# Optimization experiments

Measured on AMD Instinct MI355X. Metric: run time of the kernel, lower is better.

## Reference

```python
import jax, jax.numpy as jnp
import numpy as np

N_NODES = 50000
N_EDGES = 1600000
D = 128
LEAKY_SLOPE = 0.01  # torch nn.LeakyReLU default


def setup_inputs() -> dict:
    key = jax.random.key(0)
    ks = jax.random.split(key, 7)
    entity_embed = jax.random.normal(ks[0], (N_NODES, D), dtype=jnp.float32)
    W1 = jax.random.normal(ks[1], (D, D), dtype=jnp.float32) * 0.05
    b1 = jax.random.normal(ks[2], (D,), dtype=jnp.float32) * 0.05
    W2 = jax.random.normal(ks[3], (D, D), dtype=jnp.float32) * 0.05
    b2 = jax.random.normal(ks[4], (D,), dtype=jnp.float32) * 0.05
    src = jax.random.randint(ks[5], (N_EDGES,), 0, N_NODES, dtype=jnp.int32)
    dst = jax.random.randint(ks[6], (N_EDGES,), 0, N_NODES, dtype=jnp.int32)
    return {"entity_embed": entity_embed, "W1": W1, "b1": b1,
            "W2": W2, "b2": b2, "src": src, "dst": dst}


def reference(entity_embed, W1, b1, W2, b2, src, dst):
    # DGL update_all(copy_u('node','side'), sum('side','H')):
    # H[v] = sum over edges (u -> v) of entity_embed[u]
    n = entity_embed.shape[0]
    H = jax.ops.segment_sum(entity_embed[src], dst, num_segments=n)  # [N, D]
    # neighbors branch: LeakyReLU(W_1 @ H)
    neighbors = jax.nn.leaky_relu(H @ W1.T + b1, negative_slope=LEAKY_SLOPE)
    # interactions branch: LeakyReLU(W_2 @ (node * H))
    interactions = jax.nn.leaky_relu((entity_embed * H) @ W2.T + b2,
                                     negative_slope=LEAKY_SLOPE)
    # dropout is identity at inference
    return neighbors + interactions
```

## Files before the change

### kernel.cpp

```cpp
#include <hip/hip_runtime.h>

#define NN 50000
#define DD 128
#define SLOPE 0.01f
#define NB 782
#define BCAP 2560
#define ECH 6144
#define BST 512
#define PB 2
#define OVCAP 8192
#define HP 136

using bf16x8 = __attribute__((ext_vector_type(8))) short;
using f32x4  = __attribute__((ext_vector_type(4))) float;

__device__ inline float bflo(unsigned int w) { return __uint_as_float(w << 16); }
__device__ inline float bfhi(unsigned int w) { return __uint_as_float(w & 0xffff0000u); }
__device__ inline float sbf(short s) {
    return __uint_as_float(((unsigned int)(unsigned short)s) << 16);
}
__device__ inline unsigned int rnebf(float f) {
    unsigned int u = __float_as_uint(f);
    return (u + 0x7fffu + ((u >> 16) & 1u)) >> 16;
}
__device__ inline unsigned int pack2(float lo, float hi) {
    return rnebf(lo) | (rnebf(hi) << 16);
}
__device__ inline uint4 pack8f(const float* f) {
    uint4 o;
    o.x = pack2(f[0], f[1]); o.y = pack2(f[2], f[3]);
    o.z = pack2(f[4], f[5]); o.w = pack2(f[6], f[7]);
    return o;
}
__device__ inline void addrow(float* acc, uint4 r) {
    acc[0] += bflo(r.x); acc[1] += bfhi(r.x);
    acc[2] += bflo(r.y); acc[3] += bfhi(r.y);
    acc[4] += bflo(r.z); acc[5] += bfhi(r.z);
    acc[6] += bflo(r.w); acc[7] += bfhi(r.w);
}

__global__ __launch_bounds__(BST) void convert_bin(
    const float* __restrict__ E, const float* __restrict__ W1,
    const float* __restrict__ W2, const int* __restrict__ src,
    const int* __restrict__ dst, unsigned short* __restrict__ Ebf,
    unsigned short* __restrict__ W1b, unsigned short* __restrict__ W2b,
    int* __restrict__ gtail, unsigned int* __restrict__ stag,
    int* __restrict__ ovf_cnt, int2* __restrict__ ovf,
    int n_edges, int nbin)
{
    const int tid = threadIdx.x;

    if (blockIdx.x >= nbin) {
        const int NE8 = NN * DD / 8;
        const int NW8 = DD * DD / 8;
        int t = (blockIdx.x - nbin) * BST + tid;
        const float* s; unsigned short* d; int idx;
        if (t < NE8)                { s = E;  d = Ebf; idx = t; }
        else if (t < NE8 + NW8)     { s = W1; d = W1b; idx = t - NE8; }
        else if (t < NE8 + 2 * NW8) { s = W2; d = W2b; idx = t - NE8 - NW8; }
        else return;
        float4 a = ((const float4*)s)[(size_t)idx * 2];
        float4 b = ((const float4*)s)[(size_t)idx * 2 + 1];
        uint4 o;
        o.x = pack2(a.x, a.y); o.y = pack2(a.z, a.w);
        o.z = pack2(b.x, b.y); o.w = pack2(b.z, b.w);
        ((uint4*)d)[idx] = o;
        return;
    }

    __shared__ unsigned int srt[ECH];
    __shared__ int cnt[NB], off[NB], pos[NB], gbase[NB];
    __shared__ int wsum[BST / 64];

    const int e0 = blockIdx.x * ECH;
    const int m = min(ECH, n_edges - e0);

    for (int b = tid; b < NB; b += BST) cnt[b] = 0;
    __syncthreads();

    for (int i = tid; i < m; i += BST)
        atomicAdd(&cnt[dst[e0 + i] >> 6], 1);
    __syncthreads();

    const int lane = tid & 63, w = tid >> 6;
    int b0 = tid * PB;
    int loc[PB]; int s = 0;
    #pragma unroll
    for (int j = 0; j < PB; ++j) {
        int bb = b0 + j;
        int cv = (bb < NB) ? cnt[bb] : 0;
        loc[j] = s; s += cv;
    }
    int incl = s;
    #pragma unroll
    for (int d = 1; d < 64; d <<= 1) {
        int t2 = __shfl_up(incl, d);
        if (lane >= d) incl += t2;
    }
    if (lane == 63) wsum[w] = incl;
    __syncthreads();
    int wbase = 0;
    for (int w2 = 0; w2 < w; ++w2) wbase += wsum[w2];
    int base = wbase + incl - s;
    #pragma unroll
    for (int j = 0; j < PB; ++j) {
        int bb = b0 + j;
        if (bb < NB) { off[bb] = base + loc[j]; pos[bb] = base + loc[j]; }
    }
    __syncthreads();

    for (int i = tid; i < m; i += BST) {
        int v = dst[e0 + i];
        int u = src[e0 + i];
        int bb = v >> 6;
        int p = atomicAdd(&pos[bb], 1);
        srt[p] = (unsigned int)u | ((unsigned int)(v & 63) << 16)
               | ((unsigned int)bb << 22);
    }
    __syncthreads();

    for (int bb = tid; bb < NB; bb += BST) {
        int c = cnt[bb];
        if (c) gbase[bb] = atomicAdd(&gtail[bb], c);
    }
    __syncthreads();

    for (int i = tid; i < m; i += BST) {
        unsigned int r = srt[i];
        int bb = (int)(r >> 22);
        int gp = gbase[bb] + (i - off[bb]);
        if (gp < BCAP) {
            stag[(size_t)bb * BCAP + gp] = r & 0x3fffffu;
        } else {
            int oi = atomicAdd(ovf_cnt, 1);
            if (oi < OVCAP)
                ovf[oi] = make_int2((int)(r & 0xffffu),
                                    bb * 64 + (int)((r >> 16) & 63));
        }
    }
}

__global__ __launch_bounds__(512) void bucket_fused(
    const unsigned short* __restrict__ Ebf, const int* __restrict__ gtail,
    const unsigned int* __restrict__ stag, const int* __restrict__ ovf_cnt,
    const int2* __restrict__ ovf,
    const unsigned short* __restrict__ W1b, const unsigned short* __restrict__ W2b,
    const float* __restrict__ b1, const float* __restrict__ b2,
    float* __restrict__ out)
{
    __shared__ unsigned short sorted[BCAP];
    __shared__ unsigned short Hs[64][HP];
    __shared__ int cnt[64], off[65], pos[64];
    __shared__ int s_novf;

    const int b = blockIdx.x;
    const int tid = threadIdx.x;
    int len = gtail[b]; len = len < BCAP ? len : BCAP;
    const unsigned int* seg = stag + (size_t)b * BCAP;

    if (tid == 0) { int t = *ovf_cnt; s_novf = t < OVCAP ? t : OVCAP; }
    if (tid < 64) cnt[tid] = 0;
    __syncthreads();
    for (int i = tid; i < len; i += 512)
        atomicAdd(&cnt[(seg[i] >> 16) & 63], 1);
    __syncthreads();
    if (tid == 0) {
        int a = 0;
        for (int j = 0; j < 64; ++j) { off[j] = a; pos[j] = a; a += cnt[j]; }
        off[64] = a;
    }
    __syncthreads();
    for (int i = tid; i < len; i += 512) {
        unsigned int r = seg[i];
        int p = atomicAdd(&pos[(r >> 16) & 63], 1);
        sorted[p] = (unsigned short)(r & 0xffffu);
    }
    __syncthreads();
    const int novf = s_novf;

    const int g = tid >> 4;
    const int c = tid & 15;
    const uint4* E4 = (const uint4*)Ebf;
    for (int p2 = 0; p2 < 2; ++p2) {
        int nl = p2 * 32 + g;
        int v = b * 64 + nl;
        if (v >= NN) continue;
        float acc[8] = {};
        int i = off[nl], e1 = off[nl + 1];
        for (; i + 8 <= e1; i += 8) {
            uint4 r0 = E4[(size_t)sorted[i]     * 16 + c];
            uint4 r1 = E4[(size_t)sorted[i + 1] * 16 + c];
            uint4 r2 = E4[(size_t)sorted[i + 2] * 16 + c];
            uint4 r3 = E4[(size_t)sorted[i + 3] * 16 + c];
            uint4 r4 = E4[(size_t)sorted[i + 4] * 16 + c];
            uint4 r5 = E4[(size_t)sorted[i + 5] * 16 + c];
            uint4 r6 = E4[(size_t)sorted[i + 6] * 16 + c];
            uint4 r7 = E4[(size_t)sorted[i + 7] * 16 + c];
            addrow(acc, r0); addrow(acc, r1); addrow(acc, r2); addrow(acc, r3);
            addrow(acc, r4); addrow(acc, r5); addrow(acc, r6); addrow(acc, r7);
        }
        for (; i + 2 <= e1; i += 2) {
            uint4 r0 = E4[(size_t)sorted[i]     * 16 + c];
            uint4 r1 = E4[(size_t)sorted[i + 1] * 16 + c];
            addrow(acc, r0); addrow(acc, r1);
        }
        if (i < e1) addrow(acc, E4[(size_t)sorted[i] * 16 + c]);

        if (novf > 0) {
            for (int k = 0; k < novf; ++k) {
                int2 e = ovf[k];
                if (e.y == v) addrow(acc, E4[(size_t)e.x * 16 + c]);
            }
        }
        *(uint4*)&Hs[nl][c * 8] = pack8f(acc);
    }
    __syncthreads();

    const int wave = tid >> 6;
    const int lane = tid & 63;
    const int rw = wave >> 1;
    const int ch = wave & 1;
    const int v0 = b * 64 + rw * 16;
    if (v0 >= NN) return;
    const int m = lane & 15;
    const int quad = lane >> 4;

    bf16x8 aH[4], aE[4];
    const unsigned short* hrow = &Hs[rw * 16 + m][quad * 8];
    const unsigned short* erow = Ebf + (size_t)(v0 + m) * DD + quad * 8;
    #pragma unroll
    for (int ks = 0; ks < 4; ++ks) {
        bf16x8 h8 = *(const bf16x8*)(hrow + ks * 32);
        bf16x8 e8 = *(const bf16x8*)(erow + ks * 32);
        aH[ks] = h8;
        bf16x8 eh;
        #pragma unroll
        for (int j = 0; j < 8; ++j)
            eh[j] = (short)rnebf(sbf(h8[j]) * sbf(e8[j]));
        aE[ks] = eh;
    }

    #pragma unroll
    for (int jt = ch * 4; jt < ch * 4 + 4; ++jt) {
        const int j0 = jt * 16;
        const unsigned short* w1r = W1b + (size_t)(j0 + m) * DD + quad * 8;
        const unsigned short* w2r = W2b + (size_t)(j0 + m) * DD + quad * 8;
        f32x4 acc1 = {0.f, 0.f, 0.f, 0.f}, acc2 = {0.f, 0.f, 0.f, 0.f};
        #pragma unroll
        for (int ks = 0; ks < 4; ++ks) {
            bf16x8 bw1 = *(const bf16x8*)(w1r + ks * 32);
            bf16x8 bw2 = *(const bf16x8*)(w2r + ks * 32);
            acc1 = __builtin_amdgcn_mfma_f32_16x16x32_bf16(aH[ks], bw1, acc1, 0, 0, 0);
            acc2 = __builtin_amdgcn_mfma_f32_16x16x32_bf16(aE[ks], bw2, acc2, 0, 0, 0);
        }
        const float bb1 = b1[j0 + m], bb2 = b2[j0 + m];
        #pragma unroll
        for (int i = 0; i < 4; ++i) {
            int row = v0 + quad * 4 + i;
            if (row < NN) {
                float x1 = acc1[i] + bb1; x1 = x1 > 0.f ? x1 : SLOPE * x1;
                float x2 = acc2[i] + bb2; x2 = x2 > 0.f ? x2 : SLOPE * x2;
                out[(size_t)row * DD + j0 + m] = x1 + x2;
            }
        }
    }
}

__global__ __launch_bounds__(256) void scatter_add(
    const float* __restrict__ E, const int* __restrict__ src,
    const int* __restrict__ dst, float* __restrict__ H, int n_edges)
{
    int t = blockIdx.x * 256 + threadIdx.x;
    int e = t >> 5;
    if (e >= n_edges) return;
    int c = t & 31;
    float4 a = ((const float4*)E)[(size_t)src[e] * 32 + c];
    float* hp = H + (size_t)dst[e] * DD + c * 4;
    atomicAdd(hp + 0, a.x); atomicAdd(hp + 1, a.y);
    atomicAdd(hp + 2, a.z); atomicAdd(hp + 3, a.w);
}

__global__ __launch_bounds__(256) void fused_mlp(
    const float* __restrict__ E, const float* __restrict__ H,
    const float* __restrict__ W1, const float* __restrict__ b1,
    const float* __restrict__ W2, const float* __restrict__ b2,
    float* __restrict__ out)
{
    __shared__ float Hsf[32][DD];
    __shared__ float EHs[32][DD];
    __shared__ float W1s[DD][20];
    __shared__ float W2s[DD][20];
    const int tid = threadIdx.x;
    const int v0 = blockIdx.x * 32;
    const int nvalid = min(32, NN - v0);
    for (int i = 0; i < 4; ++i) {
        int f = tid + 256 * i;
        int n = f >> 5, c = f & 31;
        float4 h = make_float4(0.f, 0.f, 0.f, 0.f);
        float4 eh = h;
        if (n < nvalid) {
            h = ((const float4*)H)[(size_t)(v0 + n) * 32 + c];
            float4 e4 = ((const float4*)E)[(size_t)(v0 + n) * 32 + c];
            eh = make_float4(e4.x * h.x, e4.y * h.y, e4.z * h.z, e4.w * h.w);
        }
        *((float4*)&Hsf[n][c * 4]) = h;
        *((float4*)&EHs[n][c * 4]) = eh;
    }
    const int jg = tid & 63;
    const int n0 = (tid >> 6) * 8;
    float acc1a[8] = {}, acc1b[8] = {}, acc2a[8] = {}, acc2b[8] = {};
    for (int t8 = 0; t8 < 8; ++t8) {
        const int k0 = t8 * 16;
        __syncthreads();
        for (int i = 0; i < 8; ++i) {
            int f = tid + 256 * i;
            int j = f >> 4, kk = f & 15;
            W1s[j][kk] = W1[j * DD + k0 + kk];
            W2s[j][kk] = W2[j * DD + k0 + kk];
        }
        __syncthreads();
        for (int c = 0; c < 4; ++c) {
            float4 w1a = *((const float4*)&W1s[jg][c * 4]);
            float4 w1b = *((const float4*)&W1s[jg + 64][c * 4]);
            float4 w2a = *((const float4*)&W2s[jg][c * 4]);
            float4 w2b = *((const float4*)&W2s[jg + 64][c * 4]);
            const int kk = k0 + c * 4;
            for (int n = 0; n < 8; ++n) {
                float4 h = *((const float4*)&Hsf[n0 + n][kk]);
                float4 eh = *((const float4*)&EHs[n0 + n][kk]);
                acc1a[n] += h.x * w1a.x + h.y * w1a.y + h.z * w1a.z + h.w * w1a.w;
                acc1b[n] += h.x * w1b.x + h.y * w1b.y + h.z * w1b.z + h.w * w1b.w;
                acc2a[n] += eh.x * w2a.x + eh.y * w2a.y + eh.z * w2a.z + eh.w * w2a.w;
                acc2b[n] += eh.x * w2b.x + eh.y * w2b.y + eh.z * w2b.z + eh.w * w2b.w;
            }
        }
    }
    const float b1a = b1[jg], b1b = b1[jg + 64];
    const float b2a = b2[jg], b2b = b2[jg + 64];
    for (int n = 0; n < 8; ++n) {
        if (n0 + n < nvalid) {
            const int v = v0 + n0 + n;
            float x1 = acc1a[n] + b1a; x1 = x1 > 0.f ? x1 : SLOPE * x1;
            float x2 = acc2a[n] + b2a; x2 = x2 > 0.f ? x2 : SLOPE * x2;
            out[(size_t)v * DD + jg] = x1 + x2;
            float y1 = acc1b[n] + b1b; y1 = y1 > 0.f ? y1 : SLOPE * y1;
            float y2 = acc2b[n] + b2b; y2 = y2 > 0.f ? y2 : SLOPE * y2;
            out[(size_t)v * DD + jg + 64] = y1 + y2;
        }
    }
}

extern "C" void kernel_launch(void* const* d_in, const int* in_sizes, int n_in,
                              void* d_out, int out_size, void* d_ws, size_t ws_size,
                              hipStream_t stream)
{
    const float* E  = (const float*)d_in[0];
    const float* W1 = (const float*)d_in[1];
    const float* b1 = (const float*)d_in[2];
    const float* W2 = (const float*)d_in[3];
    const float* b2 = (const float*)d_in[4];
    const int* src  = (const int*)d_in[5];
    const int* dst  = (const int*)d_in[6];
    float* out = (float*)d_out;
    const int n_edges = in_sizes[5];

    char* ws = (char*)d_ws;
    auto al = [](size_t x) { return (x + 255) & ~(size_t)255; };

    const size_t off_tail = 0;
    const size_t off_ovfc = (size_t)NB * 4;
    const size_t off_ovf  = al(off_ovfc + 4);
    const size_t off_stag = al(off_ovf + (size_t)OVCAP * 8);
    const size_t off_Ebf  = al(off_stag + (size_t)NB * BCAP * 4);
    const size_t off_W1b  = al(off_Ebf + (size_t)NN * DD * 2);
    const size_t off_W2b  = al(off_W1b + (size_t)DD * DD * 2);
    const size_t need_bf  = off_W2b + (size_t)DD * DD * 2;

    if (ws_size >= need_bf) {
        int*  gtail   = (int*)(ws + off_tail);
        int*  ovf_cnt = (int*)(ws + off_ovfc);
        int2* ovf     = (int2*)(ws + off_ovf);
        unsigned int*   stag = (unsigned int*)(ws + off_stag);
        unsigned short* Ebf  = (unsigned short*)(ws + off_Ebf);
        unsigned short* W1b  = (unsigned short*)(ws + off_W1b);
        unsigned short* W2b  = (unsigned short*)(ws + off_W2b);

        const int nbin = (n_edges + ECH - 1) / ECH;
        const int ncv  = NN * DD / 8 + 2 * (DD * DD / 8);
        const int ncvb = (ncv + BST - 1) / BST;

        hipMemsetAsync(ws, 0, off_ovf, stream);
        convert_bin<<<nbin + ncvb, BST, 0, stream>>>(
            E, W1, W2, src, dst, Ebf, W1b, W2b,
            gtail, stag, ovf_cnt, ovf, n_edges, nbin);
        bucket_fused<<<NB, 512, 0, stream>>>(
            Ebf, gtail, stag, ovf_cnt, ovf, W1b, W2b, b1, b2, out);
        return;
    }

    const size_t hbytes = (size_t)NN * DD * sizeof(float);
    float* H = (ws_size >= hbytes) ? (float*)ws : out;
    hipMemsetAsync(H, 0, hbytes, stream);
    scatter_add<<<((n_edges * 32) + 255) / 256, 256, 0, stream>>>(
        E, src, dst, H, n_edges);
    fused_mlp<<<(NN + 31) / 32, 256, 0, stream>>>(E, H, W1, b1, W2, b2, out);
}
```

Baseline: 191.2 us.

## Split convert and binning kernels, halve bucket block size, parallel-scan offsets

Splits the combined convert/bin kernel into two separate launches: a 256-thread bf16 conversion kernel and an edge-binning kernel. The fused bucket kernel drops to 256 threads with launch bounds targeting 4 blocks per CU. Each wave now handles 16 rows across all 8 output tiles, and the gather phase covers 4 node groups per thread with a sched_barrier separating the loads from the accumulation. The serial 64-entry prefix sum is replaced by a wave shuffle scan. The goal is better occupancy and load overlap, at the cost of an extra launch and losing the concurrency between conversion and binning.

```diff
diff --git a/kernel.cpp b/kernel.cpp
--- a/kernel.cpp
+++ b/kernel.cpp
@@ -39,39 +39,38 @@
     acc[6] += bflo(r.w); acc[7] += bfhi(r.w);
 }
 
-__global__ __launch_bounds__(BST) void convert_bin(
+__global__ __launch_bounds__(256) void convert_bf(
     const float* __restrict__ E, const float* __restrict__ W1,
-    const float* __restrict__ W2, const int* __restrict__ src,
-    const int* __restrict__ dst, unsigned short* __restrict__ Ebf,
-    unsigned short* __restrict__ W1b, unsigned short* __restrict__ W2b,
+    const float* __restrict__ W2, unsigned short* __restrict__ Ebf,
+    unsigned short* __restrict__ W1b, unsigned short* __restrict__ W2b)
+{
+    const int NE8 = NN * DD / 8;
+    const int NW8 = DD * DD / 8;
+    int t = blockIdx.x * 256 + threadIdx.x;
+    const float* s; unsigned short* d; int idx;
+    if (t < NE8)                { s = E;  d = Ebf; idx = t; }
+    else if (t < NE8 + NW8)     { s = W1; d = W1b; idx = t - NE8; }
+    else if (t < NE8 + 2 * NW8) { s = W2; d = W2b; idx = t - NE8 - NW8; }
+    else return;
+    float4 a = ((const float4*)s)[(size_t)idx * 2];
+    float4 b = ((const float4*)s)[(size_t)idx * 2 + 1];
+    uint4 o;
+    o.x = pack2(a.x, a.y); o.y = pack2(a.z, a.w);
+    o.z = pack2(b.x, b.y); o.w = pack2(b.z, b.w);
+    ((uint4*)d)[idx] = o;
+}
+
+__global__ __launch_bounds__(BST) void bin_edges(
+    const int* __restrict__ src, const int* __restrict__ dst,
     int* __restrict__ gtail, unsigned int* __restrict__ stag,
     int* __restrict__ ovf_cnt, int2* __restrict__ ovf,
-    int n_edges, int nbin)
-{
-    const int tid = threadIdx.x;
-
-    if (blockIdx.x >= nbin) {
-        const int NE8 = NN * DD / 8;
-        const int NW8 = DD * DD / 8;
-        int t = (blockIdx.x - nbin) * BST + tid;
-        const float* s; unsigned short* d; int idx;
-        if (t < NE8)                { s = E;  d = Ebf; idx = t; }
-        else if (t < NE8 + NW8)     { s = W1; d = W1b; idx = t - NE8; }
-        else if (t < NE8 + 2 * NW8) { s = W2; d = W2b; idx = t - NE8 - NW8; }
-        else return;
-        float4 a = ((const float4*)s)[(size_t)idx * 2];
-        float4 b = ((const float4*)s)[(size_t)idx * 2 + 1];
-        uint4 o;
-        o.x = pack2(a.x, a.y); o.y = pack2(a.z, a.w);
-        o.z = pack2(b.x, b.y); o.w = pack2(b.z, b.w);
-        ((uint4*)d)[idx] = o;
-        return;
-    }
-
+    int n_edges)
+{
     __shared__ unsigned int srt[ECH];
     __shared__ int cnt[NB], off[NB], pos[NB], gbase[NB];
     __shared__ int wsum[BST / 64];
 
+    const int tid = threadIdx.x;
     const int e0 = blockIdx.x * ECH;
     const int m = min(ECH, n_edges - e0);
 
@@ -140,7 +139,7 @@
     }
 }
 
-__global__ __launch_bounds__(512) void bucket_fused(
+__global__ __launch_bounds__(256, 4) void bucket_fused(
     const unsigned short* __restrict__ Ebf, const int* __restrict__ gtail,
     const unsigned int* __restrict__ stag, const int* __restrict__ ovf_cnt,
     const int2* __restrict__ ovf,
@@ -161,16 +160,23 @@
     if (tid == 0) { int t = *ovf_cnt; s_novf = t < OVCAP ? t : OVCAP; }
     if (tid < 64) cnt[tid] = 0;
     __syncthreads();
-    for (int i = tid; i < len; i += 512)
+    for (int i = tid; i < len; i += 256)
         atomicAdd(&cnt[(seg[i] >> 16) & 63], 1);
     __syncthreads();
-    if (tid == 0) {
-        int a = 0;
-        for (int j = 0; j < 64; ++j) { off[j] = a; pos[j] = a; a += cnt[j]; }
-        off[64] = a;
-    }
-    __syncthreads();
-    for (int i = tid; i < len; i += 512) {
+    if (tid < 64) {
+        int cv = cnt[tid];
+        int incl = cv;
+        #pragma unroll
+        for (int d = 1; d < 64; d <<= 1) {
+            int t2 = __shfl_up(incl, d);
+            if (tid >= d) incl += t2;
+        }
+        off[tid] = incl - cv;
+        pos[tid] = incl - cv;
+        if (tid == 63) off[64] = incl;
+    }
+    __syncthreads();
+    for (int i = tid; i < len; i += 256) {
         unsigned int r = seg[i];
         int p = atomicAdd(&pos[(r >> 16) & 63], 1);
         sorted[p] = (unsigned short)(r & 0xffffu);
@@ -181,23 +187,20 @@
     const int g = tid >> 4;
     const int c = tid & 15;
     const uint4* E4 = (const uint4*)Ebf;
-    for (int p2 = 0; p2 < 2; ++p2) {
-        int nl = p2 * 32 + g;
+    for (int p4 = 0; p4 < 4; ++p4) {
+        int nl = p4 * 16 + g;
         int v = b * 64 + nl;
         if (v >= NN) continue;
         float acc[8] = {};
         int i = off[nl], e1 = off[nl + 1];
+        uint4 r[8];
         for (; i + 8 <= e1; i += 8) {
-            uint4 r0 = E4[(size_t)sorted[i]     * 16 + c];
-            uint4 r1 = E4[(size_t)sorted[i + 1] * 16 + c];
-            uint4 r2 = E4[(size_t)sorted[i + 2] * 16 + c];
-            uint4 r3 = E4[(size_t)sorted[i + 3] * 16 + c];
-            uint4 r4 = E4[(size_t)sorted[i + 4] * 16 + c];
-            uint4 r5 = E4[(size_t)sorted[i + 5] * 16 + c];
-            uint4 r6 = E4[(size_t)sorted[i + 6] * 16 + c];
-            uint4 r7 = E4[(size_t)sorted[i + 7] * 16 + c];
-            addrow(acc, r0); addrow(acc, r1); addrow(acc, r2); addrow(acc, r3);
-            addrow(acc, r4); addrow(acc, r5); addrow(acc, r6); addrow(acc, r7);
+            #pragma unroll
+            for (int k = 0; k < 8; ++k)
+                r[k] = E4[(size_t)sorted[i + k] * 16 + c];
+            __builtin_amdgcn_sched_barrier(0);
+            #pragma unroll
+            for (int k = 0; k < 8; ++k) addrow(acc, r[k]);
         }
         for (; i + 2 <= e1; i += 2) {
             uint4 r0 = E4[(size_t)sorted[i]     * 16 + c];
@@ -218,15 +221,13 @@
 
     const int wave = tid >> 6;
     const int lane = tid & 63;
-    const int rw = wave >> 1;
-    const int ch = wave & 1;
-    const int v0 = b * 64 + rw * 16;
+    const int v0 = b * 64 + wave * 16;
     if (v0 >= NN) return;
     const int m = lane & 15;
     const int quad = lane >> 4;
 
     bf16x8 aH[4], aE[4];
-    const unsigned short* hrow = &Hs[rw * 16 + m][quad * 8];
+    const unsigned short* hrow = &Hs[wave * 16 + m][quad * 8];
     const unsigned short* erow = Ebf + (size_t)(v0 + m) * DD + quad * 8;
     #pragma unroll
     for (int ks = 0; ks < 4; ++ks) {
@@ -241,7 +242,7 @@
     }
 
     #pragma unroll
-    for (int jt = ch * 4; jt < ch * 4 + 4; ++jt) {
+    for (int jt = 0; jt < 8; ++jt) {
         const int j0 = jt * 16;
         const unsigned short* w1r = W1b + (size_t)(j0 + m) * DD + quad * 8;
         const unsigned short* w2r = W2b + (size_t)(j0 + m) * DD + quad * 8;
@@ -387,13 +388,13 @@
 
         const int nbin = (n_edges + ECH - 1) / ECH;
         const int ncv  = NN * DD / 8 + 2 * (DD * DD / 8);
-        const int ncvb = (ncv + BST - 1) / BST;
+        const int ncvb = (ncv + 255) / 256;
 
         hipMemsetAsync(ws, 0, off_ovf, stream);
-        convert_bin<<<nbin + ncvb, BST, 0, stream>>>(
-            E, W1, W2, src, dst, Ebf, W1b, W2b,
-            gtail, stag, ovf_cnt, ovf, n_edges, nbin);
-        bucket_fused<<<NB, 512, 0, stream>>>(
+        convert_bf<<<ncvb, 256, 0, stream>>>(E, W1, W2, Ebf, W1b, W2b);
+        bin_edges<<<nbin, BST, 0, stream>>>(
+            src, dst, gtail, stag, ovf_cnt, ovf, n_edges);
+        bucket_fused<<<NB, 256, 0, stream>>>(
             Ebf, gtail, stag, ovf_cnt, ovf, W1b, W2b, b1, b2, out);
         return;
     }
```

Result: no change. 191.5 us (+0.1%).
